# Kernel tuning notes

Hardware: AMD Instinct MI355X
Metric: run time of the kernel (lower is better)

The kernel has to match this reference:

```python
import jax, jax.numpy as jnp
import numpy as np

B, S, D = 2, 2048, 2048
H, KVH, HD = 16, 4, 128
M = 2  # modalities
THETA = 10000.0
REP = H // KVH


def make_freq_cis(seq_len, head_dim, theta):
    # (S, head_dim//2, 2, 2) rotation matrices [[cos,-sin],[sin,cos]]
    inv = theta ** (-jnp.arange(0, head_dim, 2, dtype=jnp.float32) / head_dim)
    ang = jnp.arange(seq_len, dtype=jnp.float32)[:, None] * inv[None, :]  # (S, hd/2)
    c, s = jnp.cos(ang), jnp.sin(ang)
    row0 = jnp.stack([c, -s], axis=-1)
    row1 = jnp.stack([s, c], axis=-1)
    return jnp.stack([row0, row1], axis=-2)  # (S, hd/2, 2, 2)


def setup_inputs() -> dict:
    key = jax.random.key(0)
    ks = jax.random.split(key, 7)
    std = D ** -0.5
    x = jax.random.normal(ks[0], (B, S, D), dtype=jnp.float32)
    freq_cis = make_freq_cis(S, HD, THETA)
    modality_ids = jax.random.randint(ks[1], (B, S), 0, M, dtype=jnp.int32)
    wq = jax.random.normal(ks[2], (M, D, H * HD), dtype=jnp.float32) * std
    wk = jax.random.normal(ks[3], (M, D, KVH * HD), dtype=jnp.float32) * std
    wv = jax.random.normal(ks[4], (M, D, KVH * HD), dtype=jnp.float32) * std
    wo = jax.random.normal(ks[5], (M, H * HD, D), dtype=jnp.float32) * std
    return {"x": x, "freq_cis": freq_cis, "modality_ids": modality_ids,
            "wq": wq, "wk": wk, "wv": wv, "wo": wo}


def apply_rope(t, freq_cis):
    # t: (B, S, h, HD); freq_cis: (S, HD//2, 2, 2)
    b, s, h, hd = t.shape
    t2 = t.reshape(b, s, h, hd // 2, 2)
    out = jnp.einsum('bshdk,sdjk->bshdj', t2, freq_cis)
    return out.reshape(b, s, h, hd)


def reference(x, freq_cis, modality_ids, wq, wk, wv, wo):
    bsz, seq, dim = x.shape
    onehot = jax.nn.one_hot(modality_ids, M, dtype=x.dtype)  # (B,S,M)
    # per-modality QKV projection, then combine (masks partition tokens)
    q = jnp.einsum('bsm,bsd,mdo->bso', onehot, x, wq).reshape(bsz, seq, H, HD)
    k = jnp.einsum('bsm,bsd,mdo->bso', onehot, x, wk).reshape(bsz, seq, KVH, HD)
    v = jnp.einsum('bsm,bsd,mdo->bso', onehot, x, wv).reshape(bsz, seq, KVH, HD)
    q = apply_rope(q, freq_cis)
    k = apply_rope(k, freq_cis)
    # GQA: repeat_interleave kv heads along head dim
    k = jnp.repeat(k, REP, axis=2)
    v = jnp.repeat(v, REP, axis=2)
    scale = 1.0 / jnp.sqrt(jnp.asarray(HD, dtype=x.dtype))
    scores = jnp.einsum('bqhd,bkhd->bhqk', q, k) * scale
    causal = jnp.tril(jnp.ones((seq, seq), dtype=bool))
    scores = jnp.where(causal[None, None], scores, jnp.finfo(x.dtype).min)
    probs = jax.nn.softmax(scores, axis=-1)
    attn = jnp.einsum('bhqk,bkhd->bqhd', probs, v).reshape(bsz, seq, H * HD)
    # per-modality output projection
    out = jnp.einsum('bsm,bso,moe->bse', onehot, attn, wo)
    return out
```

## Files before the change

kernel.cpp:

```cpp
#include <hip/hip_runtime.h>
#include <stdint.h>

typedef unsigned short u16;
typedef __bf16  bf16x8 __attribute__((ext_vector_type(8), may_alias));
typedef u16     u16x8  __attribute__((ext_vector_type(8), may_alias));
typedef float   f32x4  __attribute__((ext_vector_type(4)));
typedef float   f32x4u __attribute__((ext_vector_type(4), may_alias));

#define Bv   2
#define Sv   2048
#define Dv   2048
#define Hv   16
#define KVHv 4
#define HDv  128
#define Tv   (Bv*Sv)
#define QKVN 3072
#define MAXROWS 4352

__device__ __forceinline__ float b2f(u16 u) {
    union { float f; uint32_t i; } x; x.i = ((uint32_t)u) << 16; return x.f;
}
__device__ __forceinline__ u16 f2b(float f) {
    union { float f; uint32_t u; } x; x.f = f;
    uint32_t r = x.u + 0x7fff + ((x.u >> 16) & 1);
    return (u16)(r >> 16);
}
__device__ __forceinline__ void gload_lds16(const void* g, void* l) {
    __builtin_amdgcn_global_load_lds((__attribute__((address_space(1))) void*)(uintptr_t)g,
                                     (__attribute__((address_space(3))) void*)(uintptr_t)l,
                                     16, 0, 0);
}

__global__ __launch_bounds__(1024) void scan_mod(const int* __restrict__ mod, int* __restrict__ fwd,
                                                 int* __restrict__ inv, int* __restrict__ hdr) {
    __shared__ int cnt[1024];
    const int tid = threadIdx.x;
    int m[4]; int c = 0;
#pragma unroll
    for (int e = 0; e < 4; ++e) { m[e] = mod[tid * 4 + e]; c += (m[e] == 0); }
    cnt[tid] = c;
    __syncthreads();
    for (int off = 1; off < 1024; off <<= 1) {
        int v = (tid >= off) ? cnt[tid - off] : 0;
        __syncthreads();
        cnt[tid] += v;
        __syncthreads();
    }
    const int c0 = cnt[1023];
    const int c0pad = (c0 + 255) & ~255;
    const int c1 = Tv - c0;
    const int total = c0pad + ((c1 + 255) & ~255);
    for (int p = tid; p < MAXROWS; p += 1024) inv[p] = -1;
    __syncthreads();
    const int ex0 = cnt[tid] - c;
    int z = 0;
#pragma unroll
    for (int e = 0; e < 4; ++e) {
        int t = tid * 4 + e;
        int pos;
        if (m[e] == 0) { pos = ex0 + z; ++z; }
        else           { pos = c0pad + (t - (ex0 + z)); }
        fwd[t] = pos;
        inv[pos] = t;
    }
    if (tid == 0) { hdr[0] = total >> 8; hdr[1] = c0pad; hdr[2] = total; }
}

__global__ void gather_cast(const float* __restrict__ x, const int* __restrict__ inv,
                            u16* __restrict__ Xg) {
    int v = blockIdx.x * 256 + threadIdx.x;
    int pos = v >> 8, c8 = (v & 255) * 8;
    int t = inv[pos];
    u16x8 val = {0, 0, 0, 0, 0, 0, 0, 0};
    if (t >= 0) {
        f32x4u a = *(const f32x4u*)&x[(size_t)t * Dv + c8];
        f32x4u b = *(const f32x4u*)&x[(size_t)t * Dv + c8 + 4];
#pragma unroll
        for (int j = 0; j < 4; ++j) { val[j] = f2b(a[j]); val[4 + j] = f2b(b[j]); }
    }
    *(u16x8*)&Xg[(size_t)pos * Dv + c8] = val;
}

__global__ void transpose_cast(const float* __restrict__ in, u16* __restrict__ out, int C,
                               size_t inZ, size_t outZ) {
    in  += (size_t)blockIdx.z * inZ;
    out += (size_t)blockIdx.z * outZ;
    __shared__ u16 tile[64][72];
    const int tr = blockIdx.y * 64, tc = blockIdx.x * 64;
    const int tid = threadIdx.x;
#pragma unroll
    for (int i = 0; i < 4; ++i) {
        int s = tid + 256 * i;
        int r = s >> 4, c4 = (s & 15) * 4;
        f32x4u v = *(const f32x4u*)&in[(size_t)(tr + r) * C + tc + c4];
#pragma unroll
        for (int j = 0; j < 4; ++j) tile[r][c4 + j] = f2b(v[j]);
    }
    __syncthreads();
#pragma unroll
    for (int i = 0; i < 2; ++i) {
        int s = tid + 256 * i;
        int r = s >> 3, c8 = (s & 7) * 8;
        u16x8 v;
#pragma unroll
        for (int j = 0; j < 8; ++j) v[j] = tile[c8 + j][r];
        *(u16x8*)&out[(size_t)(tc + r) * 2048 + tr + c8] = v;
    }
}

__device__ __forceinline__ void store_c(u16* C, size_t idx, float v) { C[idx] = f2b(v); }
__device__ __forceinline__ void store_c(float* C, size_t idx, float v) { C[idx] = v; }

template <typename OutT>
__global__ __launch_bounds__(512, 2) void gemm256(const u16* __restrict__ A,
                                                  const u16* __restrict__ Bt,
                                                  OutT* __restrict__ C,
                                                  const int* __restrict__ inv,
                                                  const int* __restrict__ hdr,
                                                  int Nfull, int ldC) {
    const int total = hdr[2], c0pad = hdr[1];
    const int bm = blockIdx.y * 256;
    if (bm >= total) return;
    const u16* B = Bt + (size_t)((bm >= c0pad) ? 1 : 0) * Nfull * 2048;
    const int bn = blockIdx.x * 256;
    const int tid = threadIdx.x;
    const int wave = tid >> 6, lane = tid & 63;
    const int l15 = lane & 15, l4 = lane >> 4;
    const int wm = wave >> 2;
    const int wn = wave & 3;
    const int bhh = wn >> 1, brr = (wn & 1) * 64;
    const int rsw = l15 & 7;
    __shared__ u16 ldsA[2][2][128 * 64];
    __shared__ u16 ldsB[2][2][128 * 64];
    const int srow = tid >> 3;
    const int ssw  = (tid & 7) ^ (srow & 7);
    const int wofs = wave * 8 * 64;

    f32x4 acc[8][4] = {};

    auto stA = [&](int sl, int h, int jrb, int kt) {
        gload_lds16(A + (size_t)(bm + h * 128 + jrb * 64 + srow) * 2048 + kt * 64 + ssw * 8,
                    &ldsA[sl][h][jrb * 64 * 64 + wofs]);
    };
    auto stB = [&](int sl, int h, int jrb, int kt) {
        gload_lds16(B + (size_t)(bn + h * 128 + jrb * 64 + srow) * 2048 + kt * 64 + ssw * 8,
                    &ldsB[sl][h][jrb * 64 * 64 + wofs]);
    };

    stB(0, 0, 0, 0); stB(0, 0, 1, 0); stB(0, 1, 0, 0); stB(0, 1, 1, 0);
    stA(0, 0, 0, 0); stA(0, 1, 0, 0); stA(0, 0, 1, 0); stA(0, 1, 1, 0);
    asm volatile("s_waitcnt vmcnt(2)" ::: "memory");
    __builtin_amdgcn_s_barrier();
    __builtin_amdgcn_sched_barrier(0);

    for (int kt = 0; kt < 32; ++kt) {
        const int s = kt & 1;
        const bool st = (kt < 31);
        bf16x8 bfr[4][2];
#pragma unroll
        for (int fj = 0; fj < 4; ++fj)
#pragma unroll
            for (int kc = 0; kc < 2; ++kc)
                bfr[fj][kc] = *(const bf16x8*)&ldsB[s][bhh][(brr + fj * 16 + l15) * 64 + ((kc * 4 + l4) ^ rsw) * 8];
#pragma unroll
        for (int q = 0; q < 4; ++q) {
            bf16x8 af[2][2];
#pragma unroll
            for (int fi = 0; fi < 2; ++fi)
#pragma unroll
                for (int kc = 0; kc < 2; ++kc)
                    af[fi][kc] = *(const bf16x8*)&ldsA[s][wm][(q * 32 + fi * 16 + l15) * 64 + ((kc * 4 + l4) ^ rsw) * 8];
            if (st) {
                if      (q == 0) { stB(s ^ 1, 0, 0, kt + 1); stB(s ^ 1, 0, 1, kt + 1); }
                else if (q == 1) { stB(s ^ 1, 1, 0, kt + 1); stB(s ^ 1, 1, 1, kt + 1); }
                else if (q == 2) { stA(s ^ 1, 0, 0, kt + 1); stA(s ^ 1, 1, 0, kt + 1); }
                else             { stA(s ^ 1, 0, 1, kt + 1); stA(s ^ 1, 1, 1, kt + 1); }
            }
            __builtin_amdgcn_s_setprio(1);
#pragma unroll
            for (int kc = 0; kc < 2; ++kc)
#pragma unroll
                for (int fi = 0; fi < 2; ++fi)
#pragma unroll
                    for (int fj = 0; fj < 4; ++fj)
                        acc[q * 2 + fi][fj] = __builtin_amdgcn_mfma_f32_16x16x32_bf16(
                            af[fi][kc], bfr[fj][kc], acc[q * 2 + fi][fj], 0, 0, 0);
            __builtin_amdgcn_s_setprio(0);
            if (q == 1) {
                if (st) asm volatile("s_waitcnt vmcnt(4)" ::: "memory");
                else    asm volatile("s_waitcnt vmcnt(0)" ::: "memory");
                __builtin_amdgcn_sched_barrier(0);
            }
            if (q == 3 && st) {
                asm volatile("s_waitcnt vmcnt(2)" ::: "memory");
                __builtin_amdgcn_sched_barrier(0);
            }
            __builtin_amdgcn_s_barrier();
            __builtin_amdgcn_sched_barrier(0);
        }
    }
#pragma unroll
    for (int fi = 0; fi < 8; ++fi)
#pragma unroll
        for (int r = 0; r < 4; ++r) {
            int row = bm + wm * 128 + fi * 16 + l4 * 4 + r;
            int t = inv[row];
            if (t >= 0) {
#pragma unroll
                for (int fj = 0; fj < 4; ++fj) {
                    int col = bn + wn * 64 + fj * 16 + l15;
                    store_c(C, (size_t)t * ldC + col, acc[fi][fj][r]);
                }
            }
        }
}

__global__ void rope_kernel(u16* __restrict__ QKV, const float* __restrict__ fc) {
    int p8 = blockIdx.x * 256 + threadIdx.x;
    const int t = p8 / 160;
    const int r8 = (p8 - t * 160) * 8;
    const int s = t & (Sv - 1);
    int col, d2b; float scale;
    if (r8 < 1024) { col = 2 * r8;               d2b = r8 & 63;  scale = 0.12751742f; }
    else           { int rr = r8 - 1024; col = 2048 + 2 * rr; d2b = rr & 63; scale = 1.0f; }
    u16* ptr = QKV + (size_t)t * QKVN + col;
    u16x8 va = *(const u16x8*)ptr;
    u16x8 vb = *(const u16x8*)(ptr + 8);
    u16 arr[16];
#pragma unroll
    for (int i = 0; i < 8; ++i) { arr[i] = va[i]; arr[8 + i] = vb[i]; }
#pragma unroll
    for (int i = 0; i < 8; ++i) {
        float t0 = b2f(arr[2 * i]), t1 = b2f(arr[2 * i + 1]);
        f32x4u f = *(const f32x4u*)&fc[((size_t)s * 64 + d2b + i) * 4];
        arr[2 * i]     = f2b((t0 * f[0] + t1 * f[1]) * scale);
        arr[2 * i + 1] = f2b((t0 * f[2] + t1 * f[3]) * scale);
    }
#pragma unroll
    for (int i = 0; i < 8; ++i) { va[i] = arr[i]; vb[i] = arr[8 + i]; }
    *(u16x8*)ptr = va;
    *(u16x8*)(ptr + 8) = vb;
}

__global__ __launch_bounds__(512) void attn_fwd(const u16* __restrict__ QKV, u16* __restrict__ Ag,
                                                const int* __restrict__ fwd) {
    const int qt = 15 - blockIdx.x;
    const int h = blockIdx.y, b = blockIdx.z;
    const int kvh = h >> 2;
    const int tid = threadIdx.x, wave = tid >> 6, lane = tid & 63;
    const int l15 = lane & 15, l4 = lane >> 4;
    const int nj = 2 * qt + 2;
    __shared__ u16 smem[32768];

    bf16x8 qf[4];
    {
        const size_t qrow = (size_t)(b * Sv + qt * 128 + wave * 16 + l15);
#pragma unroll
        for (int kc = 0; kc < 4; ++kc)
            qf[kc] = *(const bf16x8*)&QKV[qrow * QKVN + h * 128 + kc * 32 + l4 * 8];
    }
    f32x4 oacc[8] = {};
    float mrow = -1e30f;
    float lrow = 0.f;

    const size_t kvbase = (size_t)b * Sv * QKVN + 2048 + kvh * 128;

    {
#pragma unroll
        for (int i = 0; i < 2; ++i) {
            int s_u = wave * 64 + 512 * i;
            int s = s_u + lane;
            int r = s >> 4;
            int kvsrc = (r & 32) | ((r & 12) << 1) | ((r & 16) >> 2) | (r & 3);
            int cs = (s & 15) ^ (r & 7);
            gload_lds16(QKV + kvbase + (size_t)kvsrc * QKVN + cs * 8, &smem[(size_t)s_u * 8]);
        }
        u16x8 vr0 = *(const u16x8*)&QKV[kvbase + 512 + (size_t)lane * QKVN + (0 * 8 + wave) * 8];
        u16x8 vr1 = *(const u16x8*)&QKV[kvbase + 512 + (size_t)lane * QKVN + (1 * 8 + wave) * 8];
#pragma unroll
        for (int jj = 0; jj < 8; ++jj) {
            int d0 = wave * 8 + jj, d1 = (8 + wave) * 8 + jj;
            smem[16384 + d0 * 64 + ((((lane >> 3) ^ jj) << 3) | (lane & 7))] = vr0[jj];
            smem[16384 + d1 * 64 + ((((lane >> 3) ^ jj) << 3) | (lane & 7))] = vr1[jj];
        }
    }
    __syncthreads();

    for (int j = 0; j < nj; ++j) {
        const int cur = j & 1;
        const bool stage_next = (j + 1 < nj);
        u16* Kcur = smem + cur * 8192;
        u16* Knxt = smem + (cur ^ 1) * 8192;
        u16* Vcur = smem + 16384 + cur * 8192;
        u16* Vnxt = smem + 16384 + (cur ^ 1) * 8192;
        u16x8 vn0, vn1;
        if (stage_next) {
            const size_t nb = kvbase + (size_t)(j + 1) * 64 * QKVN;
#pragma unroll
            for (int i = 0; i < 2; ++i) {
                int s_u = wave * 64 + 512 * i;
                int s = s_u + lane;
                int r = s >> 4;
                int kvsrc = (r & 32) | ((r & 12) << 1) | ((r & 16) >> 2) | (r & 3);
                int cs = (s & 15) ^ (r & 7);
                gload_lds16(QKV + nb + (size_t)kvsrc * QKVN + cs * 8, &Knxt[(size_t)s_u * 8]);
            }
            vn0 = *(const u16x8*)&QKV[nb + 512 + (size_t)lane * QKVN + (0 * 8 + wave) * 8];
            vn1 = *(const u16x8*)&QKV[nb + 512 + (size_t)lane * QKVN + (1 * 8 + wave) * 8];
        }
        {
            f32x4 sacc[4] = {};
#pragma unroll
            for (int kc = 0; kc < 4; ++kc)
#pragma unroll
                for (int nt = 0; nt < 4; ++nt) {
                    int cs = ((kc * 4 + l4) ^ (l15 & 7));
                    bf16x8 kf = *(const bf16x8*)&Kcur[(nt * 16 + l15) * 128 + cs * 8];
                    sacc[nt] = __builtin_amdgcn_mfma_f32_16x16x32_bf16(kf, qf[kc], sacc[nt], 0, 0, 0);
                }
            if (j >= 2 * qt) {
                const int dq = (j - 2 * qt) * 64 - (wave * 16 + l15);
#pragma unroll
                for (int nt = 0; nt < 4; ++nt)
#pragma unroll
                    for (int r = 0; r < 4; ++r)
                        if (dq + (nt >> 1) * 32 + l4 * 8 + (nt & 1) * 4 + r > 0)
                            sacc[nt][r] = -1e30f;
            }
            f32x4 mv = sacc[0];
#pragma unroll
            for (int nt = 1; nt < 4; ++nt)
#pragma unroll
                for (int r = 0; r < 4; ++r) mv[r] = fmaxf(mv[r], sacc[nt][r]);
            float mx = fmaxf(fmaxf(mv[0], mv[1]), fmaxf(mv[2], mv[3]));
            mx = fmaxf(mx, __shfl_xor(mx, 16, 64));
            mx = fmaxf(mx, __shfl_xor(mx, 32, 64));
            float mnew = fmaxf(mrow, mx);
            float fs = exp2f(mrow - mnew);
            mrow = mnew;
            f32x4 pv = {0.f, 0.f, 0.f, 0.f};
#pragma unroll
            for (int nt = 0; nt < 4; ++nt)
#pragma unroll
                for (int r = 0; r < 4; ++r) {
                    float pe = exp2f(sacc[nt][r] - mnew);
                    sacc[nt][r] = pe;
                    pv[r] += pe;
                }
            float ps = (pv[0] + pv[1]) + (pv[2] + pv[3]);
            ps += __shfl_xor(ps, 16, 64);
            ps += __shfl_xor(ps, 32, 64);
            lrow = lrow * fs + ps;
#pragma unroll
            for (int nt = 0; nt < 8; ++nt)
#pragma unroll
                for (int r = 0; r < 4; ++r) oacc[nt][r] *= fs;
            union { uint32_t w[4]; bf16x8 v; } pb0u, pb1u;
#pragma unroll
            for (int nt = 0; nt < 2; ++nt) {
                asm("v_cvt_pk_bf16_f32 %0, %1, %2" : "=v"(pb0u.w[nt * 2])     : "v"(sacc[nt][0]), "v"(sacc[nt][1]));
                asm("v_cvt_pk_bf16_f32 %0, %1, %2" : "=v"(pb0u.w[nt * 2 + 1]) : "v"(sacc[nt][2]), "v"(sacc[nt][3]));
                asm("v_cvt_pk_bf16_f32 %0, %1, %2" : "=v"(pb1u.w[nt * 2])     : "v"(sacc[nt + 2][0]), "v"(sacc[nt + 2][1]));
                asm("v_cvt_pk_bf16_f32 %0, %1, %2" : "=v"(pb1u.w[nt * 2 + 1]) : "v"(sacc[nt + 2][2]), "v"(sacc[nt + 2][3]));
            }
            bf16x8 pb0 = pb0u.v, pb1 = pb1u.v;
#pragma unroll
            for (int nt = 0; nt < 8; ++nt) {
                int d = nt * 16 + l15;
                bf16x8 v0 = *(const bf16x8*)&Vcur[d * 64 + ((l4 ^ (l15 & 7)) << 3)];
                bf16x8 v1 = *(const bf16x8*)&Vcur[d * 64 + (((4 + l4) ^ (l15 & 7)) << 3)];
                oacc[nt] = __builtin_amdgcn_mfma_f32_16x16x32_bf16(v0, pb0, oacc[nt], 0, 0, 0);
                oacc[nt] = __builtin_amdgcn_mfma_f32_16x16x32_bf16(v1, pb1, oacc[nt], 0, 0, 0);
            }
        }
        if (stage_next) {
#pragma unroll
            for (int jj = 0; jj < 8; ++jj) {
                int d0 = wave * 8 + jj, d1 = (8 + wave) * 8 + jj;
                Vnxt[d0 * 64 + ((((lane >> 3) ^ jj) << 3) | (lane & 7))] = vn0[jj];
                Vnxt[d1 * 64 + ((((lane >> 3) ^ jj) << 3) | (lane & 7))] = vn1[jj];
            }
        }
        __syncthreads();
    }
    {
        u16* epi = smem + wave * (16 * 136);
        float rinv = 1.0f / lrow;
#pragma unroll
        for (int nt = 0; nt < 8; ++nt)
#pragma unroll
            for (int r = 0; r < 4; ++r)
                epi[l15 * 136 + nt * 16 + l4 * 4 + r] = f2b(oacc[nt][r] * rinv);
        const int q = lane >> 2;
        const int rowmap = fwd[b * Sv + qt * 128 + wave * 16 + q];
#pragma unroll
        for (int it = 0; it < 4; ++it) {
            int dv = (lane & 3) + it * 4;
            u16x8 v = *(const u16x8*)&epi[q * 136 + dv * 8];
            *(u16x8*)&Ag[(size_t)rowmap * 2048 + h * 128 + dv * 8] = v;
        }
    }
}

extern "C" void kernel_launch(void* const* d_in, const int* in_sizes, int n_in,
                              void* d_out, int out_size, void* d_ws, size_t ws_size,
                              hipStream_t stream) {
    const float* x   = (const float*)d_in[0];
    const float* fc  = (const float*)d_in[1];
    const int*   mod = (const int*)d_in[2];
    const float* wq  = (const float*)d_in[3];
    const float* wk  = (const float*)d_in[4];
    const float* wv  = (const float*)d_in[5];
    const float* wo  = (const float*)d_in[6];
    float* out = (float*)d_out;
    char* ws = (char*)d_ws;
    u16* Wqkv_t = (u16*)(ws);
    u16* Wo_t   = (u16*)(ws + 25165824);
    u16* Xg     = (u16*)(ws + 41943040);
    u16* QKV    = (u16*)(ws + 59768832);
    int* fwd    = (int*)(ws + 84934656);
    int* inv    = (int*)(ws + 84951040);
    int* hdr    = (int*)(ws + 84968448);
    u16* Ag     = Xg;

    transpose_cast<<<dim3(32, 32, 2), 256, 0, stream>>>(wq, Wqkv_t, 2048,
        (size_t)2048 * 2048, (size_t)3072 * 2048);
    transpose_cast<<<dim3(8, 32, 2),  256, 0, stream>>>(wk, Wqkv_t + (size_t)2048 * 2048, 512,
        (size_t)2048 * 512,  (size_t)3072 * 2048);
    transpose_cast<<<dim3(8, 32, 2),  256, 0, stream>>>(wv, Wqkv_t + (size_t)2560 * 2048, 512,
        (size_t)2048 * 512,  (size_t)3072 * 2048);
    transpose_cast<<<dim3(32, 32, 2), 256, 0, stream>>>(wo, Wo_t, 2048,
        (size_t)2048 * 2048, (size_t)2048 * 2048);
    scan_mod<<<1, 1024, 0, stream>>>(mod, fwd, inv, hdr);
    gather_cast<<<MAXROWS, 256, 0, stream>>>(x, inv, Xg);
    gemm256<u16><<<dim3(12, 17), 512, 0, stream>>>(Xg, Wqkv_t, QKV, inv, hdr, 3072, 3072);
    rope_kernel<<<2560, 256, 0, stream>>>(QKV, fc);
    attn_fwd<<<dim3(16, 16, 2), 512, 0, stream>>>(QKV, Ag, fwd);
    gemm256<float><<<dim3(8, 17), 512, 0, stream>>>(Ag, Wo_t, out, inv, hdr, 2048, 2048);
}
```

Baseline: 263.6 us.

## Pair complementary causal query blocks per workgroup and defer softmax rescaling

Each workgroup now handles two 64-row query blocks, p and 31-p, one per group of four waves. Both groups share a single streamed K/V pipeline over all 32 key tiles, and each group skips the tiles past its causal limit. This balances causal work across workgroups and removes the tail imbalance of the old descending-qt schedule. It also adds lazy online-softmax rescaling, which skips the max update while the new max stays within 8 of the old one (log2 domain), and s_setprio around the MFMA sections. The risks are idle waves in the lower group, extra K/V loads for the short block, and a wider exponent range from the deferred max. The launch grid x dimension must change to 16 somewhere not shown here.

```diff
diff --git a/kernel.cpp b/kernel.cpp
--- a/kernel.cpp
+++ b/kernel.cpp
@@ -244,17 +244,18 @@
 
 __global__ __launch_bounds__(512) void attn_fwd(const u16* __restrict__ QKV, u16* __restrict__ Ag,
                                                 const int* __restrict__ fwd) {
-    const int qt = 15 - blockIdx.x;
+    const int p = blockIdx.x;
     const int h = blockIdx.y, b = blockIdx.z;
     const int kvh = h >> 2;
     const int tid = threadIdx.x, wave = tid >> 6, lane = tid & 63;
+    const int wgrp = wave >> 2, wl = wave & 3;
     const int l15 = lane & 15, l4 = lane >> 4;
-    const int nj = 2 * qt + 2;
+    const int myqb = wgrp ? (31 - p) : p;
     __shared__ u16 smem[32768];
 
     bf16x8 qf[4];
     {
-        const size_t qrow = (size_t)(b * Sv + qt * 128 + wave * 16 + l15);
+        const size_t qrow = (size_t)(b * Sv + myqb * 64 + wl * 16 + l15);
 #pragma unroll
         for (int kc = 0; kc < 4; ++kc)
             qf[kc] = *(const bf16x8*)&QKV[qrow * QKVN + h * 128 + kc * 32 + l4 * 8];
@@ -286,9 +287,9 @@
     }
     __syncthreads();
 
-    for (int j = 0; j < nj; ++j) {
+    for (int j = 0; j < 32; ++j) {
         const int cur = j & 1;
-        const bool stage_next = (j + 1 < nj);
+        const bool stage_next = (j < 31);
         u16* Kcur = smem + cur * 8192;
         u16* Knxt = smem + (cur ^ 1) * 8192;
         u16* Vcur = smem + 16384 + cur * 8192;
@@ -308,8 +309,9 @@
             vn0 = *(const u16x8*)&QKV[nb + 512 + (size_t)lane * QKVN + (0 * 8 + wave) * 8];
             vn1 = *(const u16x8*)&QKV[nb + 512 + (size_t)lane * QKVN + (1 * 8 + wave) * 8];
         }
-        {
+        if (j <= myqb) {
             f32x4 sacc[4] = {};
+            __builtin_amdgcn_s_setprio(1);
 #pragma unroll
             for (int kc = 0; kc < 4; ++kc)
 #pragma unroll
@@ -318,13 +320,13 @@
                     bf16x8 kf = *(const bf16x8*)&Kcur[(nt * 16 + l15) * 128 + cs * 8];
                     sacc[nt] = __builtin_amdgcn_mfma_f32_16x16x32_bf16(kf, qf[kc], sacc[nt], 0, 0, 0);
                 }
-            if (j >= 2 * qt) {
-                const int dq = (j - 2 * qt) * 64 - (wave * 16 + l15);
+            __builtin_amdgcn_s_setprio(0);
+            if (j == myqb) {
 #pragma unroll
                 for (int nt = 0; nt < 4; ++nt)
 #pragma unroll
                     for (int r = 0; r < 4; ++r)
-                        if (dq + (nt >> 1) * 32 + l4 * 8 + (nt & 1) * 4 + r > 0)
+                        if ((nt >> 1) * 32 + l4 * 8 + (nt & 1) * 4 + r > wl * 16 + l15)
                             sacc[nt][r] = -1e30f;
             }
             f32x4 mv = sacc[0];
@@ -335,26 +337,30 @@
             float mx = fmaxf(fmaxf(mv[0], mv[1]), fmaxf(mv[2], mv[3]));
             mx = fmaxf(mx, __shfl_xor(mx, 16, 64));
             mx = fmaxf(mx, __shfl_xor(mx, 32, 64));
-            float mnew = fmaxf(mrow, mx);
-            float fs = exp2f(mrow - mnew);
-            mrow = mnew;
+            const bool defer = __all(mx <= mrow + 8.0f);
+            if (!defer) {
+                float mnew = fmaxf(mrow, mx);
+                float fs = exp2f(mrow - mnew);
+                mrow = mnew;
+                lrow *= fs;
+#pragma unroll
+                for (int nt = 0; nt < 8; ++nt)
+#pragma unroll
+                    for (int r = 0; r < 4; ++r) oacc[nt][r] *= fs;
+            }
             f32x4 pv = {0.f, 0.f, 0.f, 0.f};
 #pragma unroll
             for (int nt = 0; nt < 4; ++nt)
 #pragma unroll
                 for (int r = 0; r < 4; ++r) {
-                    float pe = exp2f(sacc[nt][r] - mnew);
+                    float pe = exp2f(sacc[nt][r] - mrow);
                     sacc[nt][r] = pe;
                     pv[r] += pe;
                 }
             float ps = (pv[0] + pv[1]) + (pv[2] + pv[3]);
             ps += __shfl_xor(ps, 16, 64);
             ps += __shfl_xor(ps, 32, 64);
-            lrow = lrow * fs + ps;
-#pragma unroll
-            for (int nt = 0; nt < 8; ++nt)
-#pragma unroll
-                for (int r = 0; r < 4; ++r) oacc[nt][r] *= fs;
+            lrow += ps;
             union { uint32_t w[4]; bf16x8 v; } pb0u, pb1u;
 #pragma unroll
             for (int nt = 0; nt < 2; ++nt) {
@@ -364,6 +370,7 @@
                 asm("v_cvt_pk_bf16_f32 %0, %1, %2" : "=v"(pb1u.w[nt * 2 + 1]) : "v"(sacc[nt + 2][2]), "v"(sacc[nt + 2][3]));
             }
             bf16x8 pb0 = pb0u.v, pb1 = pb1u.v;
+            __builtin_amdgcn_s_setprio(1);
 #pragma unroll
             for (int nt = 0; nt < 8; ++nt) {
                 int d = nt * 16 + l15;
@@ -372,6 +379,7 @@
                 oacc[nt] = __builtin_amdgcn_mfma_f32_16x16x32_bf16(v0, pb0, oacc[nt], 0, 0, 0);
                 oacc[nt] = __builtin_amdgcn_mfma_f32_16x16x32_bf16(v1, pb1, oacc[nt], 0, 0, 0);
             }
+            __builtin_amdgcn_s_setprio(0);
         }
         if (stage_next) {
 #pragma unroll
@@ -392,7 +400,7 @@
             for (int r = 0; r < 4; ++r)
                 epi[l15 * 136 + nt * 16 + l4 * 4 + r] = f2b(oacc[nt][r] * rinv);
         const int q = lane >> 2;
-        const int rowmap = fwd[b * Sv + qt * 128 + wave * 16 + q];
+        const int rowmap = fwd[b * Sv + myqb * 64 + wl * 16 + q];
 #pragma unroll
         for (int it = 0; it < 4; ++it) {
             int dv = (lane & 3) + it * 4;
```

Result: faster. 232.6 us (-11.8%).
